# Optimization experiments

Measured on AMD Instinct MI355X. Metric: run time of the kernel, lower is better.

The kernel has to match this reference:

```python
import jax, jax.numpy as jnp
import numpy as np

N_HEAD = 12
ROPE_BASE = 10000.0


def rotate_half(x):
    h = x.shape[-1] // 2
    x1, x2 = x[..., :h], x[..., h:]
    return jnp.concatenate((-x2, x1), axis=-1)


def rope_cos_sin(T, head_dim, dtype):
    inv_freq = 1.0 / (ROPE_BASE ** (jnp.arange(0, head_dim, 2, dtype=jnp.float32) / head_dim))
    t = jnp.arange(T, dtype=jnp.float32)
    freqs = jnp.einsum('i,j->ij', t, inv_freq)          # [T, head_dim/2]
    emb = jnp.concatenate((freqs, freqs), axis=-1)       # [T, head_dim]
    return jnp.cos(emb).astype(dtype), jnp.sin(emb).astype(dtype)


def setup_inputs() -> dict:
    key = jax.random.key(0)
    ks = jax.random.split(key, 5)
    B, T, C = 1, 4096, 768
    return {
        'x': jax.random.normal(ks[0], (B, T, C), dtype=jnp.float32),
        'w_attn': jax.random.normal(ks[1], (C, 3 * C), dtype=jnp.float32) * (1.0 / np.sqrt(C)),
        'b_attn': jax.random.normal(ks[2], (3 * C,), dtype=jnp.float32) * 0.02,
        'w_proj': jax.random.normal(ks[3], (C, C), dtype=jnp.float32) * (1.0 / np.sqrt(C)),
        'b_proj': jax.random.normal(ks[4], (C,), dtype=jnp.float32) * 0.02,
    }


def reference(x, w_attn, b_attn, w_proj, b_proj):
    B, T, C = x.shape
    H = N_HEAD
    hd = C // H

    qkv = x @ w_attn + b_attn                            # [B, T, 3C]
    q, k, v = jnp.split(qkv, 3, axis=-1)
    q = q.reshape(B, T, H, hd)
    k = k.reshape(B, T, H, hd)
    v = v.reshape(B, T, H, hd)

    cos, sin = rope_cos_sin(T, hd, x.dtype)              # [T, hd]
    cos = cos[None, :, None, :]
    sin = sin[None, :, None, :]
    q = q * cos + rotate_half(q) * sin
    k = k * cos + rotate_half(k) * sin

    # [B, H, T, hd]
    q = q.transpose(0, 2, 1, 3)
    k = k.transpose(0, 2, 1, 3)
    v = v.transpose(0, 2, 1, 3)

    att = jnp.einsum('bhtd,bhsd->bhts', q, k) * (1.0 / np.sqrt(hd))
    causal_mask = jnp.triu(jnp.ones((T, T), dtype=bool), k=1)
    att = jnp.where(causal_mask, -jnp.inf, att)
    att = jax.nn.softmax(att, axis=-1)

    y = jnp.einsum('bhts,bhsd->bhtd', att, v)            # [B, H, T, hd]
    y = y.transpose(0, 2, 1, 3).reshape(B, T, C)
    return y @ w_proj + b_proj
```

## Files before the change

### kernel.cpp

```cpp
#include <hip/hip_runtime.h>
#include <hip/hip_bf16.h>
#include <math.h>

using bf16 = __hip_bfloat16;
typedef __bf16 bf16x8_t __attribute__((ext_vector_type(8)));
typedef float f32x4_t __attribute__((ext_vector_type(4)));

static __device__ __forceinline__ f32x4_t mfma16(bf16x8_t a, bf16x8_t b, f32x4_t c) {
    return __builtin_amdgcn_mfma_f32_16x16x32_bf16(a, b, c, 0, 0, 0);
}

#if __has_builtin(__builtin_amdgcn_exp2f)
#define EXP2F __builtin_amdgcn_exp2f
#else
#define EXP2F exp2f
#endif

static __device__ __forceinline__ void sincos_rev(float rev, float* s, float* c) {
    float f = rev - floorf(rev);
#if __has_builtin(__builtin_amdgcn_sinf) && __has_builtin(__builtin_amdgcn_cosf)
    *s = __builtin_amdgcn_sinf(f);
    *c = __builtin_amdgcn_cosf(f);
#else
    float th = f * 6.2831853071795864f;
    *s = __sinf(th); *c = __cosf(th);
#endif
}

static __device__ __forceinline__ void async16(bf16* lds, const bf16* g) {
    __builtin_amdgcn_global_load_lds(
        (const __attribute__((address_space(1))) unsigned int*)g,
        (__attribute__((address_space(3))) unsigned int*)lds, 16, 0, 0);
}

static __device__ __forceinline__ int detect_bf16(const unsigned short* u16) {
    const int lane = threadIdx.x & 63;
    int sane = 0;
#pragma unroll
    for (int j = 0; j < 4; ++j) {
        const unsigned short u = u16[2 * (lane * 4 + j)];
        const int e = (u >> 7) & 0xFF;
        if (u == 0 || (e >= 100 && e <= 150)) sane++;
    }
#pragma unroll
    for (int off = 1; off <= 32; off <<= 1) sane += __shfl_xor(sane, off);
    return (sane * 2 >= 256) ? 1 : 0;
}

static __device__ __forceinline__ float bias_at(const void* b, int i, int isbf) {
    return isbf ? __bfloat162float(((const bf16*)b)[i]) : ((const float*)b)[i];
}

static __device__ __forceinline__ void transpose_tile(
    const void* in, bf16* out, int in_ld, int out_ld, int bx, int by,
    int isbf, int perm, bf16 (*tile)[72]) {
    const int c0 = bx * 64, r0 = by * 64;
    const int tid = threadIdx.x;
    for (int c = tid; c < 512; c += 256) {
        const int r = c >> 3, co = (c & 7) << 3;
        if (isbf) {
            *reinterpret_cast<float4*>(&tile[r][co]) =
                *reinterpret_cast<const float4*>((const bf16*)in + (size_t)(r0 + r) * in_ld + c0 + co);
        } else {
            const float* f = (const float*)in + (size_t)(r0 + r) * in_ld + c0 + co;
            const float4 a = *reinterpret_cast<const float4*>(f);
            const float4 b = *reinterpret_cast<const float4*>(f + 4);
            tile[r][co + 0] = __float2bfloat16(a.x); tile[r][co + 1] = __float2bfloat16(a.y);
            tile[r][co + 2] = __float2bfloat16(a.z); tile[r][co + 3] = __float2bfloat16(a.w);
            tile[r][co + 4] = __float2bfloat16(b.x); tile[r][co + 5] = __float2bfloat16(b.y);
            tile[r][co + 6] = __float2bfloat16(b.z); tile[r][co + 7] = __float2bfloat16(b.w);
        }
    }
    __syncthreads();
    for (int c = tid; c < 512; c += 256) {
        const int r = c >> 3, co = (c & 7) << 3;
        union { float4 v; bf16 e[8]; } u;
#pragma unroll
        for (int j = 0; j < 8; ++j) {
            const int p = co + j;
            const int src = perm ? (((p & 3) << 4) | (p >> 2)) : p;
            u.e[j] = tile[src][r];
        }
        *reinterpret_cast<float4*>(out + (size_t)(c0 + r) * out_ld + r0 + co) = u.v;
    }
}

__global__ __launch_bounds__(256) void prep_kernel(
    const void* __restrict__ x, const void* __restrict__ w_attn,
    const void* __restrict__ w_proj, bf16* __restrict__ xb,
    bf16* __restrict__ wAT, bf16* __restrict__ wPT) {
    __shared__ bf16 tile[64][72];
    const int isbf = detect_bf16((const unsigned short*)x);
    const int b = blockIdx.x;
    if (b < 432) {
        transpose_tile(w_attn, wAT, 2304, 768, b % 36, b / 36, isbf, 0, tile);
    } else if (b < 576) {
        const int bb = b - 432;
        transpose_tile(w_proj, wPT, 768, 768, bb % 12, bb / 12, isbf, 0, tile);
    } else {
        const int i = ((b - 576) * 256 + threadIdx.x) * 8;
        if (isbf) {
            *reinterpret_cast<float4*>(xb + i) =
                *reinterpret_cast<const float4*>((const bf16*)x + i);
        } else {
            const float* f = (const float*)x + i;
            const float4 a = *reinterpret_cast<const float4*>(f);
            const float4 c = *reinterpret_cast<const float4*>(f + 4);
            union { float4 v; bf16 e[8]; } u;
            u.e[0] = __float2bfloat16(a.x); u.e[1] = __float2bfloat16(a.y);
            u.e[2] = __float2bfloat16(a.z); u.e[3] = __float2bfloat16(a.w);
            u.e[4] = __float2bfloat16(c.x); u.e[5] = __float2bfloat16(c.y);
            u.e[6] = __float2bfloat16(c.z); u.e[7] = __float2bfloat16(c.w);
            *reinterpret_cast<float4*>(xb + i) = u.v;
        }
    }
}

__global__ __launch_bounds__(256) void vt_kernel(
    const bf16* __restrict__ v, bf16* __restrict__ Vt) {
    __shared__ bf16 tile[64][72];
    transpose_tile(v, Vt, 2304, 4096, blockIdx.x, blockIdx.y, 1, 1, tile);
}

template <int MI>
__global__ __launch_bounds__(256, MI == 4 ? 3 : 4) void gemm_kernel(
    const bf16* __restrict__ A, const bf16* __restrict__ Bt,
    const void* __restrict__ bias, bf16* __restrict__ C,
    const unsigned short* __restrict__ xdet, int N, int K, int mode, int flexout) {
    constexpr int MT = MI * 32;
    __shared__ bf16 sa[MT * 64];
    __shared__ bf16 sb[128 * 64];
    const int tid = threadIdx.x, lane = tid & 63, w = tid >> 6;
    const int wm = w >> 1, wn = w & 1, quad = lane >> 4, l16 = lane & 15;
    const int m0 = blockIdx.y * MT, n0 = blockIdx.x * 128;
    const int strow = lane >> 3, stslot = lane & 7;

    const bf16* ag[MI]; const bf16* bgp[4];
#pragma unroll
    for (int i = 0; i < MI; ++i) {
        const int r = (w * MI + i) * 8 + strow;
        ag[i] = A + (size_t)(m0 + r) * K + (stslot ^ (r & 7)) * 8;
    }
#pragma unroll
    for (int i = 0; i < 4; ++i) {
        const int r = (w * 4 + i) * 8 + strow;
        bgp[i] = Bt + (size_t)(n0 + r) * K + (stslot ^ (r & 7)) * 8;
    }

    f32x4_t acc[MI][4];
#pragma unroll
    for (int i = 0; i < MI; ++i)
#pragma unroll
        for (int j = 0; j < 4; ++j) acc[i][j] = (f32x4_t){0.f, 0.f, 0.f, 0.f};

    for (int k0 = 0; k0 < K; k0 += 64) {
        __syncthreads();
#pragma unroll
        for (int i = 0; i < MI; ++i) async16(&sa[(w * MI + i) * 512], ag[i] + k0);
#pragma unroll
        for (int i = 0; i < 4; ++i)  async16(&sb[(w * 4 + i) * 512], bgp[i] + k0);
        __asm__ __volatile__("s_waitcnt vmcnt(0)" ::: "memory");
        __syncthreads();

#pragma unroll
        for (int kk = 0; kk < 2; ++kk) {
            bf16x8_t af[MI], bf_[4];
#pragma unroll
            for (int mi = 0; mi < MI; ++mi) {
                const int r = wm * (MI * 16) + mi * 16 + l16;
                af[mi] = *reinterpret_cast<const bf16x8_t*>(
                    &sa[r * 64 + (((kk * 4 + quad) ^ (r & 7)) << 3)]);
            }
#pragma unroll
            for (int ni = 0; ni < 4; ++ni) {
                const int r = wn * 64 + ni * 16 + l16;
                bf_[ni] = *reinterpret_cast<const bf16x8_t*>(
                    &sb[r * 64 + (((kk * 4 + quad) ^ (r & 7)) << 3)]);
            }
#pragma unroll
            for (int mi = 0; mi < MI; ++mi)
#pragma unroll
                for (int ni = 0; ni < 4; ++ni)
                    acc[mi][ni] = mfma16(af[mi], bf_[ni], acc[mi][ni]);
        }
    }

    const int isbf = detect_bf16(xdet);
    const int f32out = flexout && !isbf;
    const int colbase = n0 + wn * 64;
    const int rowbase = m0 + wm * (MI * 16);
    if (mode == 1 && colbase < 1536) {
        const bool isq = colbase < 768;
        const float QS = 0.18033688011112042f;
#pragma unroll
        for (int ni = 0; ni < 2; ++ni) {
            const int d = ni * 16 + l16;
            const int col_lo = colbase + d, col_hi = col_lo + 32;
            const float blo = bias_at(bias, col_lo, isbf);
            const float bhi = bias_at(bias, col_hi, isbf);
            const float invf_rev = powf(10000.0f, -(float)d * (1.0f / 32.0f)) * 0.15915494309189535f;
#pragma unroll
            for (int mi = 0; mi < MI; ++mi) {
#pragma unroll
                for (int rg = 0; rg < 4; ++rg) {
                    const int t = rowbase + mi * 16 + quad * 4 + rg;
                    float sv, cv;
                    sincos_rev((float)t * invf_rev, &sv, &cv);
                    const float lo = acc[mi][ni][rg] + blo;
                    const float hi = acc[mi][ni + 2][rg] + bhi;
                    float nlo = lo * cv - hi * sv;
                    float nhi = hi * cv + lo * sv;
                    if (isq) { nlo *= QS; nhi *= QS; }
                    C[(size_t)t * N + col_lo] = __float2bfloat16(nlo);
                    C[(size_t)t * N + col_hi] = __float2bfloat16(nhi);
                }
            }
        }
    } else {
#pragma unroll
        for (int ni = 0; ni < 4; ++ni) {
            const int col = colbase + ni * 16 + l16;
            const float b = bias_at(bias, col, isbf);
#pragma unroll
            for (int mi = 0; mi < MI; ++mi) {
#pragma unroll
                for (int rg = 0; rg < 4; ++rg) {
                    const int t = rowbase + mi * 16 + quad * 4 + rg;
                    const float v = acc[mi][ni][rg] + b;
                    if (f32out) ((float*)C)[(size_t)t * N + col] = v;
                    else        C[(size_t)t * N + col] = __float2bfloat16(v);
                }
            }
        }
    }
}

__global__ __launch_bounds__(128, 3) void attn_kernel(
    const bf16* __restrict__ qkv, const bf16* __restrict__ Vt,
    bf16* __restrict__ ybuf, bf16* __restrict__ po, float* __restrict__ pl) {
    const int h = blockIdx.y;
    const int bx = blockIdx.x;
    int qt, c, nc;
    if (bx < 16)      { qt = bx;                 c = 0;             nc = 1; }
    else if (bx < 48) { qt = 16 + (bx - 16) / 2; c = (bx - 16) % 2; nc = 2; }
    else if (bx < 96) { qt = 32 + (bx - 48) / 3; c = (bx - 48) % 3; nc = 3; }
    else              { qt = 48 + (bx - 96) / 4; c = (bx - 96) % 4; nc = 4; }
    const int kt0 = c * 16;
    const int kt1 = min(kt0 + 16, qt + 1);

    const int tid = threadIdx.x, lane = tid & 63, w = tid >> 6;
    const int quad = lane >> 4, l16 = lane & 15, sw = l16 & 7;

    __shared__ bf16 Kt[4096];
    __shared__ bf16 Vs[4096];
    __shared__ bf16 Pt[2][2][16][72];

    const int strow = lane >> 3, stslot = lane & 7;
    const bf16* kg[4]; const bf16* vg[4];
#pragma unroll
    for (int i = 0; i < 4; ++i) {
        const int ch = w * 4 + i;
        const int key = ch * 8 + strow;
        kg[i] = qkv + (size_t)key * 2304 + 768 + h * 64 + (stslot ^ (key & 7)) * 8;
        const int d = ch * 8 + strow;
        vg[i] = Vt + (size_t)(h * 64 + d) * 4096 + (stslot ^ (d & 7)) * 8;
    }

    const int qbase = qt * 64 + w * 32;
    bf16x8_t qf[2][2];
#pragma unroll
    for (int f = 0; f < 2; ++f)
#pragma unroll
        for (int kc = 0; kc < 2; ++kc)
            qf[f][kc] = *reinterpret_cast<const bf16x8_t*>(
                qkv + (size_t)(qbase + f * 16 + l16) * 2304 + h * 64 + kc * 32 + quad * 8);

    f32x4_t o[2][4];
#pragma unroll
    for (int f = 0; f < 2; ++f)
#pragma unroll
        for (int dt = 0; dt < 4; ++dt) o[f][dt] = (f32x4_t){0.f, 0.f, 0.f, 0.f};
    float l_i[2][4] = {{0.f, 0.f, 0.f, 0.f}, {0.f, 0.f, 0.f, 0.f}};

    for (int kt = kt0; kt < kt1; ++kt) {
        __syncthreads();
#pragma unroll
        for (int i = 0; i < 4; ++i) {
            async16(&Kt[(w * 4 + i) * 512], kg[i] + (size_t)kt * 64 * 2304);
            async16(&Vs[(w * 4 + i) * 512], vg[i] + (size_t)kt * 64);
        }
        __asm__ __volatile__("s_waitcnt vmcnt(0)" ::: "memory");
        __syncthreads();

        bf16x8_t kf[2][4], vf[2][4];
#pragma unroll
        for (int kc = 0; kc < 2; ++kc)
#pragma unroll
            for (int ct = 0; ct < 4; ++ct)
                kf[kc][ct] = *reinterpret_cast<const bf16x8_t*>(
                    &Kt[((ct * 16 + l16) << 6) + (((kc * 4 + quad) ^ sw) << 3)]);
#pragma unroll
        for (int kc = 0; kc < 2; ++kc)
#pragma unroll
            for (int dt = 0; dt < 4; ++dt)
                vf[kc][dt] = *reinterpret_cast<const bf16x8_t*>(
                    &Vs[((dt * 16 + l16) << 6) + (((kc * 4 + quad) ^ sw) << 3)]);

        f32x4_t s[2][4];
#pragma unroll
        for (int f = 0; f < 2; ++f)
#pragma unroll
            for (int ct = 0; ct < 4; ++ct) {
                s[f][ct] = mfma16(qf[f][0], kf[0][ct], (f32x4_t){0.f, 0.f, 0.f, 0.f});
                s[f][ct] = mfma16(qf[f][1], kf[1][ct], s[f][ct]);
            }

        if (kt == qt) {
#pragma unroll
            for (int f = 0; f < 2; ++f) {
                const int rowb = qbase + f * 16 + quad * 4;
#pragma unroll
                for (int ct = 0; ct < 4; ++ct) {
                    const int key = kt * 64 + ct * 16 + l16;
#pragma unroll
                    for (int rg = 0; rg < 4; ++rg)
                        if (key > rowb + rg) s[f][ct][rg] = -INFINITY;
                }
            }
        }

#pragma unroll
        for (int f = 0; f < 2; ++f)
#pragma unroll
            for (int ct = 0; ct < 4; ++ct)
#pragma unroll
                for (int rg = 0; rg < 4; ++rg) {
                    const float p = EXP2F(s[f][ct][rg]);
                    s[f][ct][rg] = p;
                    l_i[f][rg] += p;
                }

#pragma unroll
        for (int f = 0; f < 2; ++f)
#pragma unroll
            for (int rg = 0; rg < 4; ++rg) {
                union { int2 v; __hip_bfloat162 h2[2]; } pk;
                pk.h2[0] = __float22bfloat162_rn(float2{s[f][0][rg], s[f][1][rg]});
                pk.h2[1] = __float22bfloat162_rn(float2{s[f][2][rg], s[f][3][rg]});
                *reinterpret_cast<int2*>(&Pt[w][f][quad * 4 + rg][l16 * 4]) = pk.v;
            }
        __asm__ __volatile__("s_waitcnt lgkmcnt(0)" ::: "memory");

#pragma unroll
        for (int f = 0; f < 2; ++f)
#pragma unroll
            for (int kc = 0; kc < 2; ++kc) {
                const bf16x8_t pf =
                    *reinterpret_cast<const bf16x8_t*>(&Pt[w][f][l16][kc * 32 + quad * 8]);
#pragma unroll
                for (int dt = 0; dt < 4; ++dt)
                    o[f][dt] = mfma16(pf, vf[kc][dt], o[f][dt]);
            }
    }

#pragma unroll
    for (int off = 1; off <= 8; off <<= 1)
#pragma unroll
        for (int f = 0; f < 2; ++f)
#pragma unroll
            for (int rg = 0; rg < 4; ++rg) l_i[f][rg] += __shfl_xor(l_i[f][rg], off);

    if (nc == 1) {
#pragma unroll
        for (int f = 0; f < 2; ++f) {
            float linv[4];
#pragma unroll
            for (int rg = 0; rg < 4; ++rg)
                linv[rg] = (l_i[f][rg] > 0.f) ? 1.0f / l_i[f][rg] : 0.f;
#pragma unroll
            for (int dt = 0; dt < 4; ++dt)
#pragma unroll
                for (int rg = 0; rg < 4; ++rg)
                    ybuf[(size_t)(qbase + f * 16 + quad * 4 + rg) * 768 + h * 64 + dt * 16 + l16] =
                        __float2bfloat16(o[f][dt][rg] * linv[rg]);
        }
    } else {
#pragma unroll
        for (int f = 0; f < 2; ++f) {
            float linv[4];
#pragma unroll
            for (int rg = 0; rg < 4; ++rg)
                linv[rg] = (l_i[f][rg] > 0.f) ? 1.0f / l_i[f][rg] : 0.f;
#pragma unroll
            for (int dt = 0; dt < 4; ++dt)
#pragma unroll
                for (int rg = 0; rg < 4; ++rg) {
                    const int row = qbase + f * 16 + quad * 4 + rg;
                    po[((size_t)((h << 12) + row) * 4 + c) * 64 + dt * 16 + l16] =
                        __float2bfloat16(o[f][dt][rg] * linv[rg]);
                }
            if (l16 == 0) {
#pragma unroll
                for (int rg = 0; rg < 4; ++rg) {
                    const int row = qbase + f * 16 + quad * 4 + rg;
                    pl[((h << 12) + row) * 4 + c] = l_i[f][rg];
                }
            }
        }
    }
}

__global__ __launch_bounds__(256) void combine_kernel(
    const bf16* __restrict__ po, const float* __restrict__ pl,
    bf16* __restrict__ ybuf) {
    const int g = blockIdx.x * 256 + threadIdx.x;
    if (g >= 12 * 3072 * 64) return;
    const int d = g & 63;
    const int rr = (g >> 6) % 3072;
    const int h = g / (3072 * 64);
    const int r = 1024 + rr;
    const int nc = (r >> 6) / 16 + 1;
    const int base = ((h << 12) + r) * 4;
    float wsum = 0.f, acc = 0.f;
    for (int cc = 0; cc < nc; ++cc) {
        const float wgt = pl[base + cc];
        wsum += wgt;
        acc += wgt * __bfloat162float(po[(size_t)(base + cc) * 64 + d]);
    }
    ybuf[(size_t)r * 768 + h * 64 + d] = __float2bfloat16(acc / wsum);
}

extern "C" void kernel_launch(void* const* d_in, const int* in_sizes, int n_in,
                              void* d_out, int out_size, void* d_ws, size_t ws_size,
                              hipStream_t stream) {
    bf16* qkv  = (bf16*)d_ws;
    bf16* wAT  = qkv + (size_t)4096 * 2304;
    bf16* wPT  = wAT + (size_t)2304 * 768;
    bf16* Vt   = wPT + (size_t)768 * 768;
    bf16* ybuf = Vt + (size_t)768 * 4096;
    bf16* xb   = ybuf + (size_t)4096 * 768;
    bf16* po   = xb + (size_t)4096 * 768;
    float* pl  = (float*)(po + (size_t)12 * 4096 * 4 * 64);
    const unsigned short* xdet = (const unsigned short*)d_in[0];

    prep_kernel<<<2112, 256, 0, stream>>>(d_in[0], d_in[1], d_in[3], xb, wAT, wPT);
    gemm_kernel<4><<<dim3(18, 32), 256, 0, stream>>>(
        xb, wAT, d_in[2], qkv, xdet, 2304, 768, 1, 0);
    vt_kernel<<<dim3(12, 64), 256, 0, stream>>>(qkv + 1536, Vt);
    attn_kernel<<<dim3(160, 12), 128, 0, stream>>>(qkv, Vt, ybuf, po, pl);
    combine_kernel<<<9216, 256, 0, stream>>>(po, pl, ybuf);
    gemm_kernel<2><<<dim3(6, 64), 256, 0, stream>>>(
        ybuf, wPT, d_in[4], (bf16*)d_out, xdet, 768, 768, 0, 1);
}
```

Baseline: 189.2 us.

## Fuse V transpose into QKV GEMM epilogue, double-buffer K, load V directly

The QKV GEMM epilogue now writes the V slice, transposed through shared memory, straight into the Vt buffer in a permuted key order, so the separate vt_kernel launch goes away. The attention kernel double-buffers the K tile in LDS and prefetches the next tile during compute. V fragments are now read directly from global Vt instead of being staged through LDS. The output projection GEMM switches to MI=1 tiles on a larger grid. Risks are uncoalesced global V reads in the attention loop and a longer GEMM epilogue.

```diff
diff --git a/kernel.cpp b/kernel.cpp
--- a/kernel.cpp
+++ b/kernel.cpp
@@ -53,7 +53,7 @@
 
 static __device__ __forceinline__ void transpose_tile(
     const void* in, bf16* out, int in_ld, int out_ld, int bx, int by,
-    int isbf, int perm, bf16 (*tile)[72]) {
+    int isbf, bf16 (*tile)[72]) {
     const int c0 = bx * 64, r0 = by * 64;
     const int tid = threadIdx.x;
     for (int c = tid; c < 512; c += 256) {
@@ -76,11 +76,7 @@
         const int r = c >> 3, co = (c & 7) << 3;
         union { float4 v; bf16 e[8]; } u;
 #pragma unroll
-        for (int j = 0; j < 8; ++j) {
-            const int p = co + j;
-            const int src = perm ? (((p & 3) << 4) | (p >> 2)) : p;
-            u.e[j] = tile[src][r];
-        }
+        for (int j = 0; j < 8; ++j) u.e[j] = tile[co + j][r];
         *reinterpret_cast<float4*>(out + (size_t)(c0 + r) * out_ld + r0 + co) = u.v;
     }
 }
@@ -93,10 +89,10 @@
     const int isbf = detect_bf16((const unsigned short*)x);
     const int b = blockIdx.x;
     if (b < 432) {
-        transpose_tile(w_attn, wAT, 2304, 768, b % 36, b / 36, isbf, 0, tile);
+        transpose_tile(w_attn, wAT, 2304, 768, b % 36, b / 36, isbf, tile);
     } else if (b < 576) {
         const int bb = b - 432;
-        transpose_tile(w_proj, wPT, 768, 768, bb % 12, bb / 12, isbf, 0, tile);
+        transpose_tile(w_proj, wPT, 768, 768, bb % 12, bb / 12, isbf, tile);
     } else {
         const int i = ((b - 576) * 256 + threadIdx.x) * 8;
         if (isbf) {
@@ -116,20 +112,16 @@
     }
 }
 
-__global__ __launch_bounds__(256) void vt_kernel(
-    const bf16* __restrict__ v, bf16* __restrict__ Vt) {
-    __shared__ bf16 tile[64][72];
-    transpose_tile(v, Vt, 2304, 4096, blockIdx.x, blockIdx.y, 1, 1, tile);
-}
-
 template <int MI>
 __global__ __launch_bounds__(256, MI == 4 ? 3 : 4) void gemm_kernel(
     const bf16* __restrict__ A, const bf16* __restrict__ Bt,
     const void* __restrict__ bias, bf16* __restrict__ C,
-    const unsigned short* __restrict__ xdet, int N, int K, int mode, int flexout) {
+    bf16* __restrict__ VtOut, const unsigned short* __restrict__ xdet,
+    int N, int K, int mode, int flexout) {
     constexpr int MT = MI * 32;
-    __shared__ bf16 sa[MT * 64];
-    __shared__ bf16 sb[128 * 64];
+    __shared__ bf16 smem[(MT + 128) * 64];
+    bf16* sa = smem;
+    bf16* sb = smem + MT * 64;
     const int tid = threadIdx.x, lane = tid & 63, w = tid >> 6;
     const int wm = w >> 1, wn = w & 1, quad = lane >> 4, l16 = lane & 15;
     const int m0 = blockIdx.y * MT, n0 = blockIdx.x * 128;
@@ -213,6 +205,39 @@
                     if (isq) { nlo *= QS; nhi *= QS; }
                     C[(size_t)t * N + col_lo] = __float2bfloat16(nlo);
                     C[(size_t)t * N + col_hi] = __float2bfloat16(nhi);
+                }
+            }
+        }
+    } else if (mode == 1) {
+        if constexpr (MI == 4) {
+            __syncthreads();
+            bf16* T = smem + w * 2304;
+            const int vcb = colbase - 1536;
+#pragma unroll
+            for (int pass = 0; pass < 2; ++pass) {
+                if (pass) __asm__ __volatile__("s_waitcnt lgkmcnt(0)" ::: "memory");
+#pragma unroll
+                for (int nl = 0; nl < 2; ++nl) {
+                    const int ni = pass * 2 + nl;
+                    const float b = bias_at(bias, colbase + ni * 16 + l16, isbf);
+                    const int dh = nl * 16 + l16;
+#pragma unroll
+                    for (int rg = 0; rg < 4; ++rg) {
+                        union { int2 v; bf16 e[4]; } pk;
+#pragma unroll
+                        for (int mi = 0; mi < 4; ++mi)
+                            pk.e[mi] = __float2bfloat16(acc[mi][ni][rg] + b);
+                        *reinterpret_cast<int2*>(&T[dh * 72 + quad * 16 + rg * 4]) = pk.v;
+                    }
+                }
+                __asm__ __volatile__("s_waitcnt lgkmcnt(0)" ::: "memory");
+#pragma unroll
+                for (int s = 0; s < 4; ++s) {
+                    const int dh = s * 8 + (lane >> 3);
+                    const int pj = lane & 7;
+                    const float4 vv = *reinterpret_cast<const float4*>(&T[dh * 72 + pj * 8]);
+                    *reinterpret_cast<float4*>(
+                        &VtOut[(size_t)(vcb + pass * 32 + dh) * 4096 + rowbase + pj * 8]) = vv;
                 }
             }
         }
@@ -251,20 +276,17 @@
     const int tid = threadIdx.x, lane = tid & 63, w = tid >> 6;
     const int quad = lane >> 4, l16 = lane & 15, sw = l16 & 7;
 
-    __shared__ bf16 Kt[4096];
-    __shared__ bf16 Vs[4096];
+    __shared__ bf16 Kt[2][4096];
     __shared__ bf16 Pt[2][2][16][72];
 
     const int strow = lane >> 3, stslot = lane & 7;
-    const bf16* kg[4]; const bf16* vg[4];
+    const bf16* kg[4];
 #pragma unroll
     for (int i = 0; i < 4; ++i) {
-        const int ch = w * 4 + i;
-        const int key = ch * 8 + strow;
+        const int key = (w * 4 + i) * 8 + strow;
         kg[i] = qkv + (size_t)key * 2304 + 768 + h * 64 + (stslot ^ (key & 7)) * 8;
-        const int d = ch * 8 + strow;
-        vg[i] = Vt + (size_t)(h * 64 + d) * 4096 + (stslot ^ (d & 7)) * 8;
-    }
+    }
+    const bf16* vbase = Vt + (size_t)(h * 64) * 4096;
 
     const int qbase = qt * 64 + w * 32;
     bf16x8_t qf[2][2];
@@ -282,29 +304,34 @@
         for (int dt = 0; dt < 4; ++dt) o[f][dt] = (f32x4_t){0.f, 0.f, 0.f, 0.f};
     float l_i[2][4] = {{0.f, 0.f, 0.f, 0.f}, {0.f, 0.f, 0.f, 0.f}};
 
+#pragma unroll
+    for (int i = 0; i < 4; ++i)
+        async16(&Kt[0][(w * 4 + i) * 512], kg[i] + (size_t)kt0 * 64 * 2304);
+    __asm__ __volatile__("s_waitcnt vmcnt(0)" ::: "memory");
+    __syncthreads();
+
     for (int kt = kt0; kt < kt1; ++kt) {
-        __syncthreads();
-#pragma unroll
-        for (int i = 0; i < 4; ++i) {
-            async16(&Kt[(w * 4 + i) * 512], kg[i] + (size_t)kt * 64 * 2304);
-            async16(&Vs[(w * 4 + i) * 512], vg[i] + (size_t)kt * 64);
-        }
-        __asm__ __volatile__("s_waitcnt vmcnt(0)" ::: "memory");
-        __syncthreads();
-
-        bf16x8_t kf[2][4], vf[2][4];
+        const int b = (kt - kt0) & 1;
+        if (kt + 1 < kt1) {
+#pragma unroll
+            for (int i = 0; i < 4; ++i)
+                async16(&Kt[b ^ 1][(w * 4 + i) * 512], kg[i] + (size_t)(kt + 1) * 64 * 2304);
+        }
+        bf16x8_t vf[2][4];
+#pragma unroll
+        for (int kc = 0; kc < 2; ++kc)
+#pragma unroll
+            for (int dt = 0; dt < 4; ++dt)
+                vf[kc][dt] = *reinterpret_cast<const bf16x8_t*>(
+                    vbase + (size_t)(dt * 16 + l16) * 4096 + kt * 64 + kc * 32 + quad * 8);
+
+        bf16x8_t kf[2][4];
 #pragma unroll
         for (int kc = 0; kc < 2; ++kc)
 #pragma unroll
             for (int ct = 0; ct < 4; ++ct)
                 kf[kc][ct] = *reinterpret_cast<const bf16x8_t*>(
-                    &Kt[((ct * 16 + l16) << 6) + (((kc * 4 + quad) ^ sw) << 3)]);
-#pragma unroll
-        for (int kc = 0; kc < 2; ++kc)
-#pragma unroll
-            for (int dt = 0; dt < 4; ++dt)
-                vf[kc][dt] = *reinterpret_cast<const bf16x8_t*>(
-                    &Vs[((dt * 16 + l16) << 6) + (((kc * 4 + quad) ^ sw) << 3)]);
+                    &Kt[b][((ct * 16 + l16) << 6) + (((kc * 4 + quad) ^ sw) << 3)]);
 
         f32x4_t s[2][4];
 #pragma unroll
@@ -361,6 +388,9 @@
                 for (int dt = 0; dt < 4; ++dt)
                     o[f][dt] = mfma16(pf, vf[kc][dt], o[f][dt]);
             }
+
+        __asm__ __volatile__("s_waitcnt vmcnt(0)" ::: "memory");
+        __syncthreads();
     }
 
 #pragma unroll
@@ -445,10 +475,9 @@
 
     prep_kernel<<<2112, 256, 0, stream>>>(d_in[0], d_in[1], d_in[3], xb, wAT, wPT);
     gemm_kernel<4><<<dim3(18, 32), 256, 0, stream>>>(
-        xb, wAT, d_in[2], qkv, xdet, 2304, 768, 1, 0);
-    vt_kernel<<<dim3(12, 64), 256, 0, stream>>>(qkv + 1536, Vt);
+        xb, wAT, d_in[2], qkv, Vt, xdet, 2304, 768, 1, 0);
     attn_kernel<<<dim3(160, 12), 128, 0, stream>>>(qkv, Vt, ybuf, po, pl);
     combine_kernel<<<9216, 256, 0, stream>>>(po, pl, ybuf);
-    gemm_kernel<2><<<dim3(6, 64), 256, 0, stream>>>(
-        ybuf, wPT, d_in[4], (bf16*)d_out, xdet, 768, 768, 0, 1);
-}
+    gemm_kernel<1><<<dim3(6, 128), 256, 0, stream>>>(
+        ybuf, wPT, d_in[4], (bf16*)d_out, nullptr, xdet, 768, 768, 0, 1);
+}
```

Result: slower. 203.9 us (+7.8%).
